# Kernel optimization log

Measured on AMD Instinct MI355X. Metric: run time of the kernel, lower is better.

The kernel has to match this reference:

```python
import jax, jax.numpy as jnp
import numpy as np

N = 100000        # nodes
E = 1600000       # edges (avg degree 16)
H = 128           # hidden dim
LAYERS = 3
RESIDUAL = 1.0


def setup_inputs() -> dict:
    key = jax.random.key(0)
    ks = jax.random.split(key, 7)
    x = jax.random.normal(ks[0], (N, H), dtype=jnp.float32)
    src = jax.random.randint(ks[1], (E,), 0, N, dtype=jnp.int32)
    dst = jax.random.randint(ks[2], (E,), 0, N, dtype=jnp.int32)
    s = 1.0 / np.sqrt(H)
    W1 = jax.random.normal(ks[3], (H, H), dtype=jnp.float32) * s
    b1 = jnp.zeros((H,), dtype=jnp.float32)
    W2 = jax.random.normal(ks[4], (H, H), dtype=jnp.float32) * s
    b2 = jnp.zeros((H,), dtype=jnp.float32)
    return {"x": x, "src": src, "dst": dst, "W1": W1, "b1": b1, "W2": W2, "b2": b2}


def _gcn_conv(h, src, dst, dinv, W, b):
    # PyG GCNConv: h' = D^{-1/2}(A+I)D^{-1/2} (h W) + b
    h = h @ W                                   # [N,H]
    norm = dinv[src] * dinv[dst]                # [E]
    msgs = h[src] * norm[:, None]               # [E,H] gather (memory-bound)
    agg = jax.ops.segment_sum(msgs, dst, num_segments=N)  # scatter-add
    agg = agg + h * (dinv * dinv)[:, None]      # self-loop contribution
    return agg + b


def reference(x, src, dst, W1, b1, W2, b2):
    # symmetric degree normalization with self-loops (deg over dst, + 1 for self-loop)
    deg = jax.ops.segment_sum(jnp.ones((E,), x.dtype), dst, num_segments=N) + 1.0
    dinv = jax.lax.rsqrt(deg)                   # [N]

    ori = x
    h = _gcn_conv(x, src, dst, dinv, W1, b1) + RESIDUAL * ori
    for _ in range(LAYERS - 1):
        h = jax.nn.relu(h)                      # dropout is identity in eval mode
        h = _gcn_conv(h, src, dst, dinv, W2, b2) + RESIDUAL * ori
    return h
```

## Files before the change

kernel.cpp:

```cpp
#include <hip/hip_runtime.h>

#define H 128
#define AP 136
#define BSH 9
#define BSZ 512
#define MAXB 256
#define NBLK 128

typedef __attribute__((ext_vector_type(8))) short short8;
typedef __attribute__((ext_vector_type(4))) float floatx4;
typedef __attribute__((ext_vector_type(2))) float f32x2;

__device__ inline unsigned short f2b(float f) {
  union { float f; unsigned u; } v; v.f = f;
  unsigned r = v.u + 0x7fffu + ((v.u >> 16) & 1u);
  return (unsigned short)(r >> 16);
}
__device__ inline float blo(unsigned u) { return __uint_as_float(u << 16); }
__device__ inline float bhi(unsigned u) { return __uint_as_float(u & 0xffff0000u); }
__device__ inline unsigned char f2f8(float f) {
  return (unsigned char)(__builtin_amdgcn_cvt_pk_fp8_f32(f, f, 0, false) & 0xff);
}
__device__ inline f32x2 fp8x2(unsigned u) {
#if __has_builtin(__builtin_amdgcn_cvt_pk_f32_fp8)
  return __builtin_amdgcn_cvt_pk_f32_fp8(u, false);
#else
  f32x2 r;
  r.x = __builtin_amdgcn_cvt_f32_fp8(u, 0);
  r.y = __builtin_amdgcn_cvt_f32_fp8(u, 1);
  return r;
#endif
}


__global__ __launch_bounds__(256) void k_bh(const int* __restrict__ dst,
                                            int* __restrict__ bhist,
                                            int E, int NB, int chunk) {
  __shared__ int hst[MAXB];
  int tid = threadIdx.x;
  hst[tid] = 0;
  __syncthreads();
  int s = blockIdx.x * chunk;
  int eend = min(s + chunk, E);
  for (int e = s + tid; e < eend; e += 256)
    atomicAdd(&hst[dst[e] >> BSH], 1);
  __syncthreads();
  if (tid < NB) bhist[tid * NBLK + blockIdx.x] = hst[tid];
}

__global__ __launch_bounds__(256) void k_bscan(const int* __restrict__ bhist,
                                               int* __restrict__ boff2, int NB) {
  __shared__ int ps[256];
  int tid = threadIdx.x;
  int4 v[NBLK / 4];
  int sum = 0;
  if (tid < NB) {
    const int4* row = (const int4*)(bhist + tid * NBLK);
#pragma unroll
    for (int j = 0; j < NBLK / 4; j++) v[j] = row[j];
#pragma unroll
    for (int j = 0; j < NBLK / 4; j++) sum += v[j].x + v[j].y + v[j].z + v[j].w;
  }
  ps[tid] = sum;
  __syncthreads();
  for (int off = 1; off < 256; off <<= 1) {
    int t = (tid >= off) ? ps[tid - off] : 0;
    __syncthreads();
    ps[tid] += t;
    __syncthreads();
  }
  int run = ps[tid] - sum;
  if (tid < NB) {
    int4* orow = (int4*)(boff2 + tid * NBLK);
#pragma unroll
    for (int j = 0; j < NBLK / 4; j++) {
      int4 o;
      o.x = run; run += v[j].x;
      o.y = run; run += v[j].y;
      o.z = run; run += v[j].z;
      o.w = run; run += v[j].w;
      orow[j] = o;
    }
  }
}

__global__ __launch_bounds__(256) void k_bscatter(const int* __restrict__ src,
                                                  const int* __restrict__ dst,
                                                  const int* __restrict__ boff2,
                                                  int* __restrict__ bed,
                                                  int E, int NB, int chunk) {
  __shared__ int pos[MAXB];
  int tid = threadIdx.x;
  if (tid < NB) pos[tid] = boff2[tid * NBLK + blockIdx.x];
  __syncthreads();
  int s = blockIdx.x * chunk;
  int eend = min(s + chunk, E);
  for (int e = s + tid; e < eend; e += 256) {
    int d = dst[e];
    int p = atomicAdd(&pos[d >> BSH], 1);
    bed[p] = (src[e] << BSH) | (d & (BSZ - 1));
  }
}

__global__ __launch_bounds__(512) void k_build(const int* __restrict__ bed,
                                               const int* __restrict__ boff2,
                                               int* __restrict__ roff,
                                               float* __restrict__ dinv,
                                               int* __restrict__ csr,
                                               int N, int E, int NB) {
  __shared__ int cnt[BSZ];
  __shared__ int pos[BSZ];
  __shared__ int ps[BSZ];
  int b = blockIdx.x, tid = threadIdx.x;
  int bs = boff2[b * NBLK];
  int be = (b + 1 < NB) ? boff2[(b + 1) * NBLK] : E;
  int n0 = b << BSH;
  cnt[tid] = 0;
  __syncthreads();
  for (int e = bs + tid; e < be; e += 512)
    atomicAdd(&cnt[bed[e] & (BSZ - 1)], 1);
  __syncthreads();
  int c = cnt[tid];
  ps[tid] = c;
  __syncthreads();
  for (int off = 1; off < 512; off <<= 1) {
    int t = (tid >= off) ? ps[tid - off] : 0;
    __syncthreads();
    ps[tid] += t;
    __syncthreads();
  }
  int base = bs + ps[tid] - c;
  pos[tid] = base;
  int node = n0 + tid;
  if (node < N) {
    roff[node] = base;
    dinv[node] = rsqrtf((float)c + 1.0f);
  }
  __syncthreads();
  for (int e = bs + tid; e < be; e += 512) {
    int v = bed[e];
    int p = atomicAdd(&pos[v & (BSZ - 1)], 1);
    csr[p] = v >> BSH;
  }
  if (b == 0 && tid == 0) roff[N] = E;
}

__global__ __launch_bounds__(256) void k_prep(const float* __restrict__ W1,
                                              const float* __restrict__ W2,
                                              unsigned short* __restrict__ Wt1,
                                              unsigned short* __restrict__ Wt2,
                                              const float* __restrict__ x,
                                              unsigned int* __restrict__ xb, int total) {
  int tid = threadIdx.x;
  if (blockIdx.x < 2) {
    const float* W = blockIdx.x ? W2 : W1;
    unsigned short* Wt = blockIdx.x ? Wt2 : Wt1;
#pragma unroll
    for (int i = 0; i < 64; i++) {
      int idx = tid + 256 * i;
      int k = idx >> 7, n = idx & 127;
      Wt[n * 128 + k] = f2b(W[idx]);
    }
  } else {
    int i = (blockIdx.x - 2) * 256 + tid;
    if (i < total) {
      float2 v = ((const float2*)x)[i];
      xb[i] = (unsigned)f2b(v.x) | ((unsigned)f2b(v.y) << 16);
    }
  }
}

__global__ __launch_bounds__(256) void k_gemm(const unsigned int* __restrict__ in,
                                              const unsigned short* __restrict__ Wt,
                                              unsigned char* __restrict__ out,
                                              int n) {
  __shared__ short As[64 * AP];
  __shared__ short Bs[128 * AP];
  int tid = threadIdx.x;
  int wave = tid >> 6, lane = tid & 63;
  int quad = lane >> 4, l16 = lane & 15;
  int row0 = blockIdx.x * 64;

  const float4* in4 = (const float4*)in;
#pragma unroll
  for (int i = 0; i < 4; i++) {
    int idx = tid + 256 * i;
    int r = idx >> 4, c = idx & 15;
    int gr = row0 + r;
    float4 v = make_float4(0.f, 0.f, 0.f, 0.f);
    if (gr < n) v = in4[(size_t)gr * 16 + c];
    *(float4*)&As[r * AP + c * 8] = v;
  }
  const float4* Wt4 = (const float4*)Wt;
#pragma unroll
  for (int i = 0; i < 8; i++) {
    int idx = tid + 256 * i;
    int nr = idx >> 4, c = idx & 15;
    *(float4*)&Bs[nr * AP + c * 8] = Wt4[nr * 16 + c];
  }
  __syncthreads();

  floatx4 acc[4][2];
#pragma unroll
  for (int mt = 0; mt < 4; mt++)
#pragma unroll
    for (int nt = 0; nt < 2; nt++) acc[mt][nt] = (floatx4)(0.f);

#pragma unroll
  for (int ks = 0; ks < 4; ks++) {
    short8 a[4], b[2];
#pragma unroll
    for (int mt = 0; mt < 4; mt++)
      a[mt] = *(const short8*)&As[(mt * 16 + l16) * AP + ks * 32 + quad * 8];
#pragma unroll
    for (int nt = 0; nt < 2; nt++)
      b[nt] = *(const short8*)&Bs[(wave * 32 + nt * 16 + l16) * AP + ks * 32 + quad * 8];
#pragma unroll
    for (int mt = 0; mt < 4; mt++)
#pragma unroll
      for (int nt = 0; nt < 2; nt++)
        acc[mt][nt] = __builtin_amdgcn_mfma_f32_16x16x32_bf16(a[mt], b[nt], acc[mt][nt], 0, 0, 0);
  }

#pragma unroll
  for (int mt = 0; mt < 4; mt++) {
#pragma unroll
    for (int nt = 0; nt < 2; nt++) {
#pragma unroll
      for (int r = 0; r < 4; r++) {
        int gr = row0 + mt * 16 + quad * 4 + r;
        if (gr < n)
          out[(size_t)gr * H + wave * 32 + nt * 16 + l16] = f2f8(acc[mt][nt][r]);
      }
    }
  }
}

__global__ __launch_bounds__(256) void k_agg(const unsigned short* __restrict__ h,
                                             const int* __restrict__ csr,
                                             const int* __restrict__ roff,
                                             const float* __restrict__ dinv,
                                             const float* __restrict__ bias,
                                             const unsigned int* __restrict__ xb,
                                             float* __restrict__ out32,
                                             unsigned int* __restrict__ out16,
                                             int n, int write16) {
  int wave = threadIdx.x >> 6;
  int lane = threadIdx.x & 63;
  int node = blockIdx.x * 4 + wave;
  if (node >= n) return;

  float di = dinv[node];
  unsigned su = h[(size_t)node * 64 + lane];
  unsigned xu = xb[(size_t)node * 64 + lane];
  float2 bv = ((const float2*)bias)[lane];
  f32x2 sp = fp8x2(su);
  float acc0 = bv.x + blo(xu) + di * di * sp.x;
  float acc1 = bv.y + bhi(xu) + di * di * sp.y;

  int e0 = roff[node], e1 = roff[node + 1];
  int e = e0;
  for (; e + 16 <= e1; e += 16) {
    int eu = __builtin_amdgcn_readfirstlane(e);
    int idx[16];
#pragma unroll
    for (int k = 0; k < 16; k++) idx[k] = __builtin_amdgcn_readfirstlane(csr[eu + k]);
    unsigned u[16];
#pragma unroll
    for (int k = 0; k < 16; k++) u[k] = (h + ((size_t)idx[k] << 6))[lane];
    float cf[16];
#pragma unroll
    for (int k = 0; k < 16; k++) cf[k] = di * dinv[idx[k]];
#pragma unroll
    for (int k = 0; k < 16; k++) {
      f32x2 p = fp8x2(u[k]);
      acc0 += cf[k] * p.x;
      acc1 += cf[k] * p.y;
    }
  }
  for (; e + 4 <= e1; e += 4) {
    int eu = __builtin_amdgcn_readfirstlane(e);
    int idx[4];
#pragma unroll
    for (int k = 0; k < 4; k++) idx[k] = __builtin_amdgcn_readfirstlane(csr[eu + k]);
    unsigned u[4];
#pragma unroll
    for (int k = 0; k < 4; k++) u[k] = (h + ((size_t)idx[k] << 6))[lane];
    float cf[4];
#pragma unroll
    for (int k = 0; k < 4; k++) cf[k] = di * dinv[idx[k]];
#pragma unroll
    for (int k = 0; k < 4; k++) {
      f32x2 p = fp8x2(u[k]);
      acc0 += cf[k] * p.x;
      acc1 += cf[k] * p.y;
    }
  }
  for (; e < e1; e++) {
    int s = csr[e];
    float cf = di * dinv[s];
    unsigned u = h[(size_t)s * 64 + lane];
    f32x2 p = fp8x2(u);
    acc0 += cf * p.x;
    acc1 += cf * p.y;
  }
  if (write16) {
    out16[(size_t)node * 64 + lane] =
        (unsigned)f2b(fmaxf(acc0, 0.f)) | ((unsigned)f2b(fmaxf(acc1, 0.f)) << 16);
  } else {
    ((float2*)out32)[(size_t)node * 64 + lane] = make_float2(acc0, acc1);
  }
}

extern "C" void kernel_launch(void* const* d_in, const int* in_sizes, int n_in,
                              void* d_out, int out_size, void* d_ws, size_t ws_size,
                              hipStream_t stream) {
  const float* x = (const float*)d_in[0];
  const int* src = (const int*)d_in[1];
  const int* dst = (const int*)d_in[2];
  const float* W1 = (const float*)d_in[3];
  const float* b1 = (const float*)d_in[4];
  const float* W2 = (const float*)d_in[5];
  const float* b2 = (const float*)d_in[6];
  int N = in_sizes[0] / H;
  int E = in_sizes[1];
  float* out = (float*)d_out;

  char* p = (char*)d_ws;
  auto alloc = [&](size_t bytes) {
    char* q = p;
    p += (bytes + 255) & ~(size_t)255;
    return q;
  };
  int* roff = (int*)alloc((size_t)(N + 1) * 4);
  float* dinv = (float*)alloc((size_t)N * 4);
  int* csr = (int*)alloc((size_t)E * 4);
  unsigned int* xb = (unsigned int*)alloc((size_t)N * H * 2);
  unsigned char* htmp = (unsigned char*)alloc((size_t)N * H);
  unsigned int* fbuf = (unsigned int*)alloc((size_t)N * H * 2);
  unsigned short* Wt1 = (unsigned short*)alloc(128 * 128 * 2);
  unsigned short* Wt2 = (unsigned short*)alloc(128 * 128 * 2);
  int* bhist = (int*)alloc((size_t)MAXB * NBLK * 4);
  int* boff2 = (int*)alloc((size_t)MAXB * NBLK * 4);
  int* bed = (int*)alloc((size_t)E * 4);

  int NB = (N + BSZ - 1) >> BSH;
  int chunk = (E + NBLK - 1) / NBLK;

  k_bh<<<NBLK, 256, 0, stream>>>(dst, bhist, E, NB, chunk);
  k_bscan<<<1, 256, 0, stream>>>(bhist, boff2, NB);
  k_bscatter<<<NBLK, 256, 0, stream>>>(src, dst, boff2, bed, E, NB, chunk);
  k_build<<<NB, 512, 0, stream>>>(bed, boff2, roff, dinv, csr, N, E, NB);

  int xtotal = N * (H / 2);
  k_prep<<<2 + (xtotal + 255) / 256, 256, 0, stream>>>(W1, W2, Wt1, Wt2, x, xb, xtotal);

  int gb = (N + 63) / 64;
  int ab = (N + 3) / 4;

  k_gemm<<<gb, 256, 0, stream>>>(xb, Wt1, htmp, N);
  k_agg<<<ab, 256, 0, stream>>>((const unsigned short*)htmp, csr, roff, dinv, b1, xb,
                                nullptr, fbuf, N, 1);
  k_gemm<<<gb, 256, 0, stream>>>(fbuf, Wt2, htmp, N);
  k_agg<<<ab, 256, 0, stream>>>((const unsigned short*)htmp, csr, roff, dinv, b2, xb,
                                nullptr, fbuf, N, 1);
  k_gemm<<<gb, 256, 0, stream>>>(fbuf, Wt2, htmp, N);
  k_agg<<<ab, 256, 0, stream>>>((const unsigned short*)htmp, csr, roff, dinv, b2, xb,
                                out, nullptr, N, 0);
}
```

Measured before the change: 427.2 us.

## Fuse histogram with prep, double bucketing blocks, and unify agg tail loop

The weight/feature bf16 conversion is folded into the bucket-histogram launch, which removes one kernel launch and lets both pieces of independent work run at the same time. NBLK goes from 128 to 256, which doubles the parallelism of the histogram and scatter stages, and the scan is rewritten as a flat 512-thread scan over 128-entry segments. The aggregation kernel replaces its 16/4/1 remainder loops with a single 16-wide loop that clamps indices and zeroes the out-of-range coefficients. This trades redundant gathers on the tail edges for less branching and code.

```diff
diff --git a/kernel.cpp b/kernel.cpp
--- a/kernel.cpp
+++ b/kernel.cpp
@@ -5,7 +5,7 @@
 #define BSH 9
 #define BSZ 512
 #define MAXB 256
-#define NBLK 128
+#define NBLK 256
 
 typedef __attribute__((ext_vector_type(8))) short short8;
 typedef __attribute__((ext_vector_type(4))) float floatx4;
@@ -33,47 +33,73 @@
 }
 
 
-__global__ __launch_bounds__(256) void k_bh(const int* __restrict__ dst,
-                                            int* __restrict__ bhist,
-                                            int E, int NB, int chunk) {
-  __shared__ int hst[MAXB];
+__global__ __launch_bounds__(256) void k_bh_prep(const int* __restrict__ dst,
+                                                 int* __restrict__ bhist,
+                                                 int E, int NB, int chunk,
+                                                 const float* __restrict__ W1,
+                                                 const float* __restrict__ W2,
+                                                 unsigned short* __restrict__ Wt1,
+                                                 unsigned short* __restrict__ Wt2,
+                                                 const float* __restrict__ x,
+                                                 unsigned int* __restrict__ xb,
+                                                 int xtotal) {
   int tid = threadIdx.x;
-  hst[tid] = 0;
-  __syncthreads();
-  int s = blockIdx.x * chunk;
-  int eend = min(s + chunk, E);
-  for (int e = s + tid; e < eend; e += 256)
-    atomicAdd(&hst[dst[e] >> BSH], 1);
-  __syncthreads();
-  if (tid < NB) bhist[tid * NBLK + blockIdx.x] = hst[tid];
-}
-
-__global__ __launch_bounds__(256) void k_bscan(const int* __restrict__ bhist,
-                                               int* __restrict__ boff2, int NB) {
-  __shared__ int ps[256];
+  int bx = blockIdx.x;
+  if (bx < NBLK) {
+    __shared__ int hst[MAXB];
+    hst[tid] = 0;
+    __syncthreads();
+    int s = bx * chunk;
+    int eend = min(s + chunk, E);
+    for (int e = s + tid; e < eend; e += 256)
+      atomicAdd(&hst[dst[e] >> BSH], 1);
+    __syncthreads();
+    if (tid < NB) bhist[tid * NBLK + bx] = hst[tid];
+  } else if (bx < NBLK + 2) {
+    const float* W = (bx - NBLK) ? W2 : W1;
+    unsigned short* Wt = (bx - NBLK) ? Wt2 : Wt1;
+#pragma unroll
+    for (int i = 0; i < 64; i++) {
+      int idx = tid + 256 * i;
+      int k = idx >> 7, n = idx & 127;
+      Wt[n * 128 + k] = f2b(W[idx]);
+    }
+  } else {
+    int i = (bx - NBLK - 2) * 256 + tid;
+    if (i < xtotal) {
+      float2 v = ((const float2*)x)[i];
+      xb[i] = (unsigned)f2b(v.x) | ((unsigned)f2b(v.y) << 16);
+    }
+  }
+}
+
+__global__ __launch_bounds__(512) void k_bscan(const int* __restrict__ bhist,
+                                               int* __restrict__ boff2, int total) {
+  __shared__ int ps[512];
   int tid = threadIdx.x;
-  int4 v[NBLK / 4];
+  int base = tid * 128;
+  int4 v[32];
   int sum = 0;
-  if (tid < NB) {
-    const int4* row = (const int4*)(bhist + tid * NBLK);
-#pragma unroll
-    for (int j = 0; j < NBLK / 4; j++) v[j] = row[j];
-#pragma unroll
-    for (int j = 0; j < NBLK / 4; j++) sum += v[j].x + v[j].y + v[j].z + v[j].w;
+  if (base < total) {
+    const int4* row = (const int4*)(bhist + base);
+#pragma unroll
+    for (int j = 0; j < 32; j++) v[j] = row[j];
+#pragma unroll
+    for (int j = 0; j < 32; j++) sum += v[j].x + v[j].y + v[j].z + v[j].w;
   }
   ps[tid] = sum;
   __syncthreads();
-  for (int off = 1; off < 256; off <<= 1) {
+  for (int off = 1; off < 512; off <<= 1) {
     int t = (tid >= off) ? ps[tid - off] : 0;
     __syncthreads();
     ps[tid] += t;
     __syncthreads();
   }
   int run = ps[tid] - sum;
-  if (tid < NB) {
-    int4* orow = (int4*)(boff2 + tid * NBLK);
-#pragma unroll
-    for (int j = 0; j < NBLK / 4; j++) {
+  if (base < total) {
+    int4* orow = (int4*)(boff2 + base);
+#pragma unroll
+    for (int j = 0; j < 32; j++) {
       int4 o;
       o.x = run; run += v[j].x;
       o.y = run; run += v[j].y;
@@ -145,31 +171,6 @@
   if (b == 0 && tid == 0) roff[N] = E;
 }
 
-__global__ __launch_bounds__(256) void k_prep(const float* __restrict__ W1,
-                                              const float* __restrict__ W2,
-                                              unsigned short* __restrict__ Wt1,
-                                              unsigned short* __restrict__ Wt2,
-                                              const float* __restrict__ x,
-                                              unsigned int* __restrict__ xb, int total) {
-  int tid = threadIdx.x;
-  if (blockIdx.x < 2) {
-    const float* W = blockIdx.x ? W2 : W1;
-    unsigned short* Wt = blockIdx.x ? Wt2 : Wt1;
-#pragma unroll
-    for (int i = 0; i < 64; i++) {
-      int idx = tid + 256 * i;
-      int k = idx >> 7, n = idx & 127;
-      Wt[n * 128 + k] = f2b(W[idx]);
-    }
-  } else {
-    int i = (blockIdx.x - 2) * 256 + tid;
-    if (i < total) {
-      float2 v = ((const float2*)x)[i];
-      xb[i] = (unsigned)f2b(v.x) | ((unsigned)f2b(v.y) << 16);
-    }
-  }
-}
-
 __global__ __launch_bounds__(256) void k_gemm(const unsigned int* __restrict__ in,
                                               const unsigned short* __restrict__ Wt,
                                               unsigned char* __restrict__ out,
@@ -258,51 +259,29 @@
   float acc0 = bv.x + blo(xu) + di * di * sp.x;
   float acc1 = bv.y + bhi(xu) + di * di * sp.y;
 
-  int e0 = roff[node], e1 = roff[node + 1];
-  int e = e0;
-  for (; e + 16 <= e1; e += 16) {
-    int eu = __builtin_amdgcn_readfirstlane(e);
+  int e0u = __builtin_amdgcn_readfirstlane(roff[node]);
+  int e1u = __builtin_amdgcn_readfirstlane(roff[node + 1]);
+  int last = e1u - 1;
+  for (int e = e0u; e < e1u; e += 16) {
     int idx[16];
 #pragma unroll
-    for (int k = 0; k < 16; k++) idx[k] = __builtin_amdgcn_readfirstlane(csr[eu + k]);
+    for (int k = 0; k < 16; k++) {
+      int ee = min(e + k, last);
+      idx[k] = __builtin_amdgcn_readfirstlane(csr[ee]);
+    }
     unsigned u[16];
 #pragma unroll
     for (int k = 0; k < 16; k++) u[k] = (h + ((size_t)idx[k] << 6))[lane];
     float cf[16];
 #pragma unroll
-    for (int k = 0; k < 16; k++) cf[k] = di * dinv[idx[k]];
+    for (int k = 0; k < 16; k++)
+      cf[k] = (e + k <= last) ? di * dinv[idx[k]] : 0.f;
 #pragma unroll
     for (int k = 0; k < 16; k++) {
       f32x2 p = fp8x2(u[k]);
       acc0 += cf[k] * p.x;
       acc1 += cf[k] * p.y;
     }
-  }
-  for (; e + 4 <= e1; e += 4) {
-    int eu = __builtin_amdgcn_readfirstlane(e);
-    int idx[4];
-#pragma unroll
-    for (int k = 0; k < 4; k++) idx[k] = __builtin_amdgcn_readfirstlane(csr[eu + k]);
-    unsigned u[4];
-#pragma unroll
-    for (int k = 0; k < 4; k++) u[k] = (h + ((size_t)idx[k] << 6))[lane];
-    float cf[4];
-#pragma unroll
-    for (int k = 0; k < 4; k++) cf[k] = di * dinv[idx[k]];
-#pragma unroll
-    for (int k = 0; k < 4; k++) {
-      f32x2 p = fp8x2(u[k]);
-      acc0 += cf[k] * p.x;
-      acc1 += cf[k] * p.y;
-    }
-  }
-  for (; e < e1; e++) {
-    int s = csr[e];
-    float cf = di * dinv[s];
-    unsigned u = h[(size_t)s * 64 + lane];
-    f32x2 p = fp8x2(u);
-    acc0 += cf * p.x;
-    acc1 += cf * p.y;
   }
   if (write16) {
     out16[(size_t)node * 64 + lane] =
@@ -347,13 +326,14 @@
   int NB = (N + BSZ - 1) >> BSH;
   int chunk = (E + NBLK - 1) / NBLK;
 
-  k_bh<<<NBLK, 256, 0, stream>>>(dst, bhist, E, NB, chunk);
-  k_bscan<<<1, 256, 0, stream>>>(bhist, boff2, NB);
+  int xtotal = N * (H / 2);
+  int xblocks = (xtotal + 255) / 256;
+
+  k_bh_prep<<<NBLK + 2 + xblocks, 256, 0, stream>>>(dst, bhist, E, NB, chunk,
+                                                    W1, W2, Wt1, Wt2, x, xb, xtotal);
+  k_bscan<<<1, 512, 0, stream>>>(bhist, boff2, NB * NBLK);
   k_bscatter<<<NBLK, 256, 0, stream>>>(src, dst, boff2, bed, E, NB, chunk);
   k_build<<<NB, 512, 0, stream>>>(bed, boff2, roff, dinv, csr, N, E, NB);
-
-  int xtotal = N * (H / 2);
-  k_prep<<<2 + (xtotal + 255) / 256, 256, 0, stream>>>(W1, W2, Wt1, Wt2, x, xb, xtotal);
 
   int gb = (N + 63) / 64;
   int ab = (N + 3) / 4;
```

New measurement: 444.3 us. +4.0%, slower.
